# Performance work log

Measured on AMD Instinct MI355X. Metric: run time of the kernel, lower is better.

## Reference

```python
import jax, jax.numpy as jnp
import numpy as np

B, T = 256, 64
VOCAB = 10000
VIS, WORD, RNN = 1024, 512, 512


def setup_inputs() -> dict:
    key = jax.random.key(0)
    ks = jax.random.split(key, 12)
    s = 0.02
    return {
        "vis_feats": jax.random.normal(ks[0], (B, VIS), jnp.float32),
        "seqz": jax.random.randint(ks[1], (B, T), 0, VOCAB, jnp.int32),
        # learned params (x @ W convention, W: [in, out])
        "emb": jax.random.normal(ks[2], (VOCAB + 2, WORD), jnp.float32) * s,
        "W_ih": jax.random.normal(ks[3], (VIS + WORD, 4 * RNN), jnp.float32) * s,
        "W_hh": jax.random.normal(ks[4], (RNN, 4 * RNN), jnp.float32) * s,
        "b_lstm": jnp.zeros((4 * RNN,), jnp.float32),
        "vis2g_W": jax.random.normal(ks[5], (VIS, RNN), jnp.float32) * s,
        "vis2g_b": jnp.zeros((RNN,), jnp.float32),
        "w2g_W": jax.random.normal(ks[6], (WORD, RNN), jnp.float32) * s,
        "h2g_W": jax.random.normal(ks[7], (RNN, RNN), jnp.float32) * s,
        "out_W": jax.random.normal(ks[8], (RNN, VOCAB + 1), jnp.float32) * s,
        "out_b": jnp.zeros((VOCAB + 1,), jnp.float32),
    }


def _decode(vis_feats, seqz, emb, W_ih, W_hh, b_lstm, vis2g_W, vis2g_b,
            w2g_W, h2g_W, out_W, out_b):
    Bn, Tn = seqz.shape
    # input word ids per step: SOS (=vocab+1) at t=0, then seqz[:, t-1]
    sos = jnp.full((1, Bn), VOCAB + 1, seqz.dtype)
    words = jnp.concatenate([sos, seqz[:, :-1].T], axis=0)          # [T, B]
    mask = jnp.concatenate([jnp.ones((1, Bn), jnp.float32),
                            (seqz[:, :-1] != 0).T.astype(jnp.float32)], axis=0)  # [T, B]
    targets = seqz.T                                                 # [T, B]

    def step(carry, xs):
        h, c = carry
        widx, tgt, m = xs
        w = emb[widx]                                   # [B, 512]
        x = jnp.concatenate([vis_feats, w], axis=1)     # [B, 1536]
        gates = x @ W_ih + h @ W_hh + b_lstm            # [B, 2048]
        i_g, f_g, g_g, o_g = jnp.split(gates, 4, axis=1)
        c_new = jax.nn.sigmoid(f_g) * c + jax.nn.sigmoid(i_g) * jnp.tanh(g_g)
        h_new = jax.nn.sigmoid(o_g) * jnp.tanh(c_new)
        # visual-sentinel gate: g = sigmoid(w2g(w) + vis2g(vis) + h2g(h_prev))
        g = jax.nn.sigmoid(w @ w2g_W + vis_feats @ vis2g_W + vis2g_b + h @ h2g_W)
        s_t = g * jnp.tanh(c_new)                       # [B, 512]
        logits = s_t @ out_W + out_b                    # [B, V+1]
        lp = jax.nn.log_softmax(logits, axis=-1) * m[:, None]
        out_t = jnp.take_along_axis(lp, tgt[:, None], axis=1)[:, 0]  # [B]
        return (h_new, c_new), out_t

    init = (jnp.zeros((Bn, RNN), jnp.float32), jnp.zeros((Bn, RNN), jnp.float32))
    _, log_probs = jax.lax.scan(step, init, (words, targets, mask))
    return log_probs  # [T, B]


def reference(vis_feats, seqz, emb, W_ih, W_hh, b_lstm, vis2g_W, vis2g_b,
              w2g_W, h2g_W, out_W, out_b):
    return _decode(vis_feats, seqz, emb, W_ih, W_hh, b_lstm, vis2g_W,
                   vis2g_b, w2g_W, h2g_W, out_W, out_b)
```

## Files before the change

### kernel.cpp

```cpp
#include <hip/hip_runtime.h>
#include <hip/hip_bf16.h>
#include <math.h>

typedef __attribute__((ext_vector_type(8))) short short8;
typedef __attribute__((ext_vector_type(4))) float f32x4;

#define MFMA16(a, b, c) __builtin_amdgcn_mfma_f32_16x16x32_bf16((a), (b), (c), 0, 0, 0)

#define BB 256
#define TT 64
#define VOCAB 10000
#define WORD 512
#define RNN 512
#define NC 2560
#define NV 10001
#define NVP 10016
#define NTILES 626

typedef unsigned long long ull;
union U16 { ull u[2]; short8 s8; };

__device__ __forceinline__ float sigf(float x) { return 1.f / (1.f + __expf(-x)); }
__device__ __forceinline__ float bf2f(short s) {
    union { unsigned int u; float f; } v;
    v.u = ((unsigned int)(unsigned short)s) << 16;
    return v.f;
}
__device__ __forceinline__ short f2bfs(float x) {
    __hip_bfloat16 h = __float2bfloat16(x);
    return *reinterpret_cast<short*>(&h);
}

__device__ __forceinline__ void gload_lds16(const void* g, void* l) {
    __builtin_amdgcn_global_load_lds((const __attribute__((address_space(1))) void*)g,
                                     (__attribute__((address_space(3))) void*)l, 16, 0, 0);
}

__device__ __forceinline__ void stage_tile(const short8* gsrc, void* lbuf, int w, int lane) {
    const char* g = (const char*)gsrc + w * 4096 + lane * 16;
    char* l = (char*)lbuf + w * 4096;
#pragma unroll
    for (int i = 0; i < 4; i++) gload_lds16(g + i * 1024, l + i * 1024);
}


__global__ void transpose_cvt(const float* __restrict__ src, int K, int N, int ld,
                              __hip_bfloat16* __restrict__ dst, int dst_ld, int dstN) {
    __shared__ float tile[32][33];
    int k0 = blockIdx.y * 32, n0 = blockIdx.x * 32;
    int tx = threadIdx.x, ty = threadIdx.y;
#pragma unroll
    for (int i = 0; i < 32; i += 8) {
        int k = k0 + ty + i, n = n0 + tx;
        tile[ty + i][tx] = (k < K && n < N) ? src[(size_t)k * ld + n] : 0.f;
    }
    __syncthreads();
#pragma unroll
    for (int i = 0; i < 32; i += 8) {
        int n = n0 + ty + i, k = k0 + tx;
        if (n < dstN && k < K) dst[(size_t)n * dst_ld + k] = __float2bfloat16(tile[tx][ty + i]);
    }
}

__global__ void swizzle_frag(const short8* __restrict__ src, short8* __restrict__ dst, int ntiles) {
    int t = blockIdx.x * 256 + threadIdx.x;
    if (t >= ntiles * 1024) return;
    int ct = t >> 10, r = t & 1023, kt = r >> 6, l = r & 63;
    int li = l & 15, q = l >> 4;
    dst[t] = src[(size_t)(ct * 16 + li) * 64 + kt * 4 + q];
}

__global__ void zero_state(float* c, __hip_bfloat16* h) {
    int idx = blockIdx.x * 256 + threadIdx.x;
    c[idx] = 0.f;
    h[idx] = __float2bfloat16(0.f);
}

__global__ void cvt_vis(const float* __restrict__ v, __hip_bfloat16* __restrict__ d) {
    int idx = blockIdx.x * 256 + threadIdx.x;
    d[idx] = __float2bfloat16(v[idx]);
}

__global__ __launch_bounds__(256) void gemm_vis(const __hip_bfloat16* __restrict__ A,
                                                const __hip_bfloat16* __restrict__ Bt,
                                                const float* __restrict__ b_lstm,
                                                const float* __restrict__ vis2g_b,
                                                float* __restrict__ C) {
    int wid = blockIdx.x * 4 + (threadIdx.x >> 6);
    int mt = wid / 160, nt = wid % 160;
    int lane = threadIdx.x & 63, li = lane & 15, q = lane >> 4;
    const short8* Ap = (const short8*)A + (mt * 16 + li) * 128 + q;
    const short8* Bp = (const short8*)Bt + (nt * 16 + li) * 128 + q;
    f32x4 acc = {0.f, 0.f, 0.f, 0.f};
#pragma unroll
    for (int kk = 0; kk < 128; kk += 4) acc = MFMA16(Ap[kk], Bp[kk], acc);
    int col = nt * 16 + li;
    float bias = (col < 2048) ? b_lstm[col] : vis2g_b[col - 2048];
#pragma unroll
    for (int r = 0; r < 4; r++) {
        int row = mt * 16 + q * 4 + r;
        C[row * NC + col] = acc[r] + bias;
    }
}

__global__ __launch_bounds__(256) void pre_gemm(const int* __restrict__ seqz,
                                                const float* __restrict__ emb,
                                                const short8* __restrict__ Bsw,
                                                const float* __restrict__ visC,
                                                __hip_bfloat16* __restrict__ preF) {
    __shared__ short8 lds[2][1024];
    int w = threadIdx.x >> 6, lane = threadIdx.x & 63, li = lane & 15, q = lane >> 4;
    int r0 = blockIdx.x * 128 + w * 32;

    short8 a0[16], a1[16];
    {
        int row = r0 + li;
        int t = row >> 8, b = row & 255;
        int wid_ = (t == 0) ? (VOCAB + 1) : seqz[b * TT + (t - 1)];
        const float* er = emb + (size_t)wid_ * WORD + q * 8;
#pragma unroll
        for (int kt = 0; kt < 16; kt++) {
            float4 f0 = ((const float4*)(er + kt * 32))[0];
            float4 f1 = ((const float4*)(er + kt * 32))[1];
            short8 v; v[0]=f2bfs(f0.x); v[1]=f2bfs(f0.y); v[2]=f2bfs(f0.z); v[3]=f2bfs(f0.w);
            v[4]=f2bfs(f1.x); v[5]=f2bfs(f1.y); v[6]=f2bfs(f1.z); v[7]=f2bfs(f1.w);
            a0[kt] = v;
        }
        row = r0 + 16 + li; t = row >> 8; b = row & 255;
        wid_ = (t == 0) ? (VOCAB + 1) : seqz[b * TT + (t - 1)];
        er = emb + (size_t)wid_ * WORD + q * 8;
#pragma unroll
        for (int kt = 0; kt < 16; kt++) {
            float4 f0 = ((const float4*)(er + kt * 32))[0];
            float4 f1 = ((const float4*)(er + kt * 32))[1];
            short8 v; v[0]=f2bfs(f0.x); v[1]=f2bfs(f0.y); v[2]=f2bfs(f0.z); v[3]=f2bfs(f0.w);
            v[4]=f2bfs(f1.x); v[5]=f2bfs(f1.y); v[6]=f2bfs(f1.z); v[7]=f2bfs(f1.w);
            a1[kt] = v;
        }
    }

    int t0 = blockIdx.y * 20, t1 = t0 + 20;
    stage_tile(Bsw + (size_t)t0 * 1024, lds[0], w, lane);
    int ib = 0;
    for (int ct = t0; ct < t1; ++ct, ib ^= 1) {
        __syncthreads();
        if (ct + 1 < t1) stage_tile(Bsw + (size_t)(ct + 1) * 1024, lds[ib ^ 1], w, lane);
        const short8* B = lds[ib];
        f32x4 c0 = {0.f,0.f,0.f,0.f}, c1 = {0.f,0.f,0.f,0.f};
#pragma unroll
        for (int kt = 0; kt < 16; kt++) {
            short8 bv = B[kt * 64 + lane];
            c0 = MFMA16(bv, a0[kt], c0);
            c1 = MFMA16(bv, a1[kt], c1);
        }
        int col0 = ct * 16 + q * 4;
        size_t tb0 = ((size_t)(r0 >> 4) * 160 + ct) * 256 + lane * 4;
        size_t tb1 = tb0 + (size_t)160 * 256;
        float4 v0 = *(const float4*)(visC + ((r0 + li) & 255) * NC + col0);
        float4 v1 = *(const float4*)(visC + ((r0 + 16 + li) & 255) * NC + col0);
        preF[tb0 + 0] = __float2bfloat16(c0[0] + v0.x);
        preF[tb0 + 1] = __float2bfloat16(c0[1] + v0.y);
        preF[tb0 + 2] = __float2bfloat16(c0[2] + v0.z);
        preF[tb0 + 3] = __float2bfloat16(c0[3] + v0.w);
        preF[tb1 + 0] = __float2bfloat16(c1[0] + v1.x);
        preF[tb1 + 1] = __float2bfloat16(c1[1] + v1.y);
        preF[tb1 + 2] = __float2bfloat16(c1[2] + v1.z);
        preF[tb1 + 3] = __float2bfloat16(c1[3] + v1.w);
    }
}

__global__ __launch_bounds__(64, 1) void lstm_persist(const short8* __restrict__ WHsw,
                                                      const __hip_bfloat16* __restrict__ preF,
                                                      __hip_bfloat16* __restrict__ h0,
                                                      __hip_bfloat16* __restrict__ h1,
                                                      __hip_bfloat16* __restrict__ S,
                                                      int* __restrict__ flags) {
    __shared__ short8 ldsB[4096];
    int wid = blockIdx.x;
    int bt = wid & 15, jt = (wid >> 4) & 31;
    int lane = threadIdx.x;
    int li = lane & 15, q = lane >> 4;

#pragma unroll
    for (int g = 0; g < 4; ++g) {
        const char* src = (const char*)(WHsw + (size_t)(g * 32 + jt) * 1024) + lane * 16;
        char* dst = (char*)ldsB + g * 16384;
#pragma unroll
        for (int i = 0; i < 16; ++i) gload_lds16(src + i * 1024, dst + i * 1024);
    }
    short8 b4[16];
    const short8* B4 = WHsw + (size_t)(128 + jt) * 1024 + lane;
#pragma unroll
    for (int kt = 0; kt < 16; ++kt) b4[kt] = B4[kt * 64];
    __syncthreads();

    int* flagp = flags + bt * 64;
    f32x4 cacc = {0.f, 0.f, 0.f, 0.f};

    int hin  = (bt * 16 + li) * 1024 + q * 16;
    int hout = (bt * 16 + li) * 1024 + (jt * 16 + q * 4) * 2;

    const ull* ppw = (const ull*)preF + ((size_t)bt * 160 + jt) * 64 + lane;

    ull ppA[5], ppB[5];
#pragma unroll
    for (int g = 0; g < 5; ++g) ppA[g] = ppw[g * 2048];

#define LSTM_STEP(T, HC, HN, PPC, PPN)                                             \
  {                                                                                \
    if ((T) > 0) {                                                                 \
      int it = 0;                                                                  \
      while (true) {                                                               \
        int v = (T);                                                               \
        if (lane < 32)                                                             \
          v = __hip_atomic_load(flagp + lane, __ATOMIC_RELAXED,                    \
                                __HIP_MEMORY_SCOPE_SYSTEM);                        \
        if (__all(v >= (T))) break;                                                \
        if (++it > 30000) break;               \
        __builtin_amdgcn_s_sleep(1);                                               \
      }                                                                            \
    }                                                                              \
    const ull* hp = (const ull*)((const char*)(HC) + hin);                         \
    ull hf[32];                                                                    \
    _Pragma("unroll") for (int kt = 0; kt < 16; ++kt) {                            \
      hf[2 * kt]     = __hip_atomic_load(hp + kt * 8, __ATOMIC_RELAXED,            \
                                         __HIP_MEMORY_SCOPE_SYSTEM);               \
      hf[2 * kt + 1] = __hip_atomic_load(hp + kt * 8 + 1, __ATOMIC_RELAXED,        \
                                         __HIP_MEMORY_SCOPE_SYSTEM);               \
    }                                                                              \
    if ((T) + 1 < TT) {                                                            \
      const ull* pn = ppw + (size_t)((T) + 1) * 163840;                            \
      _Pragma("unroll") for (int g = 0; g < 5; ++g) (PPN)[g] = pn[g * 2048];       \
    }                                                                              \
    f32x4 g0 = {0.f, 0.f, 0.f, 0.f}, g1 = g0, g2 = g0, g3 = g0, g4 = g0;           \
    _Pragma("unroll") for (int kt = 0; kt < 16; ++kt) {                            \
      U16 hv; hv.u[0] = hf[2 * kt]; hv.u[1] = hf[2 * kt + 1];                      \
      short8 bv = hv.s8;                                                           \
      g0 = MFMA16(ldsB[       kt * 64 + lane], bv, g0);                            \
      g1 = MFMA16(ldsB[1024 + kt * 64 + lane], bv, g1);                            \
      g2 = MFMA16(ldsB[2048 + kt * 64 + lane], bv, g2);                            \
      g3 = MFMA16(ldsB[3072 + kt * 64 + lane], bv, g3);                            \
      g4 = MFMA16(b4[kt], bv, g4);                                                 \
    }                                                                              \
    ull hvout = 0ull, svout = 0ull;                                                \
    _Pragma("unroll") for (int r = 0; r < 4; ++r) {                                \
      float ig = sigf(g0[r] + bf2f((short)((PPC)[0] >> (16 * r))));                \
      float fg = sigf(g1[r] + bf2f((short)((PPC)[1] >> (16 * r))));                \
      float gg = tanhf(g2[r] + bf2f((short)((PPC)[2] >> (16 * r))));               \
      float og = sigf(g3[r] + bf2f((short)((PPC)[3] >> (16 * r))));                \
      float gp = sigf(g4[r] + bf2f((short)((PPC)[4] >> (16 * r))));                \
      float cn = fg * cacc[r] + ig * gg;                                           \
      float tc = tanhf(cn);                                                        \
      cacc[r] = cn;                                                                \
      hvout |= ((ull)(unsigned short)f2bfs(og * tc)) << (16 * r);                  \
      svout |= ((ull)(unsigned short)f2bfs(gp * tc)) << (16 * r);                  \
    }                                                                              \
    __hip_atomic_store((ull*)((char*)(HN) + hout), hvout,                          \
                       __ATOMIC_RELAXED, __HIP_MEMORY_SCOPE_SYSTEM);               \
    *(ull*)((char*)S + (size_t)(T) * 262144 + hout) = svout;                       \
    asm volatile("s_waitcnt vmcnt(0)" ::: "memory");                               \
    if (lane == 0)                                                                 \
      __hip_atomic_store(flagp + jt, (T) + 1, __ATOMIC_RELAXED,                    \
                         __HIP_MEMORY_SCOPE_SYSTEM);                               \
  }

    for (int t = 0; t < TT; t += 2) {
        LSTM_STEP(t,     h0, h1, ppA, ppB);
        LSTM_STEP(t + 1, h1, h0, ppB, ppA);
    }
#undef LSTM_STEP
}


__global__ __launch_bounds__(256) void lse_gemm(const short8* __restrict__ S8,
                                                const short8* __restrict__ Bsw,
                                                const float* __restrict__ ob,
                                                float* __restrict__ sumexp) {
    __shared__ short8 lds[2][1024];
    int w = threadIdx.x >> 6, lane = threadIdx.x & 63, li = lane & 15, q = lane >> 4;
    int r0 = blockIdx.x * 128 + w * 32;
    short8 a0[16], a1[16];
    const short8* Sp0 = S8 + (size_t)(r0 + li) * 64 + q;
    const short8* Sp1 = S8 + (size_t)(r0 + 16 + li) * 64 + q;
#pragma unroll
    for (int kt = 0; kt < 16; kt++) { a0[kt] = Sp0[kt * 4]; a1[kt] = Sp1[kt * 4]; }

    float s0[4] = {0.f,0.f,0.f,0.f}, s1[4] = {0.f,0.f,0.f,0.f};
    int t0 = blockIdx.y * 40;
    int t1 = t0 + 40 < NTILES ? t0 + 40 : NTILES;

    stage_tile(Bsw + (size_t)t0 * 1024, lds[0], w, lane);
    int ib = 0;
    for (int ct = t0; ct < t1; ++ct, ib ^= 1) {
        __syncthreads();
        if (ct + 1 < t1) stage_tile(Bsw + (size_t)(ct + 1) * 1024, lds[ib ^ 1], w, lane);
        const short8* B = lds[ib];
        f32x4 c0 = {0.f,0.f,0.f,0.f}, c1 = {0.f,0.f,0.f,0.f};
#pragma unroll
        for (int kt = 0; kt < 16; kt++) {
            short8 bv = B[kt * 64 + lane];
            c0 = MFMA16(a0[kt], bv, c0);
            c1 = MFMA16(a1[kt], bv, c1);
        }
        int col = ct * 16 + li;
        if (col < NV) {
            float obv = ob[col];
#pragma unroll
            for (int r = 0; r < 4; r++) {
                s0[r] += __expf(c0[r] + obv);
                s1[r] += __expf(c1[r] + obv);
            }
        }
    }
#pragma unroll
    for (int off = 1; off < 16; off <<= 1) {
#pragma unroll
        for (int r = 0; r < 4; r++) { s0[r] += __shfl_xor(s0[r], off); s1[r] += __shfl_xor(s1[r], off); }
    }
    if (li == 0) {
#pragma unroll
        for (int r = 0; r < 4; r++) {
            atomicAdd(&sumexp[r0 + q * 4 + r], s0[r]);
            atomicAdd(&sumexp[r0 + 16 + q * 4 + r], s1[r]);
        }
    }
}

__global__ __launch_bounds__(256) void finalize_k(const __hip_bfloat16* __restrict__ S,
                                                  const __hip_bfloat16* __restrict__ Wt,
                                                  const float* __restrict__ ob,
                                                  const int* __restrict__ seqz,
                                                  const float* __restrict__ sumexp,
                                                  float* __restrict__ out) {
    int w = threadIdx.x >> 6, lane = threadIdx.x & 63;
    int row = blockIdx.x * 4 + w;
    int t = row >> 8, b = row & 255;
    int tgt = seqz[b * TT + t];
    short8 sv = ((const short8*)(S + (size_t)row * 512))[lane];
    short8 wv = ((const short8*)(Wt + (size_t)tgt * 512))[lane];
    float d = 0.f;
#pragma unroll
    for (int i = 0; i < 8; i++) d += bf2f(sv[i]) * bf2f(wv[i]);
#pragma unroll
    for (int off = 1; off < 64; off <<= 1) d += __shfl_xor(d, off);
    if (lane == 0) {
        bool mk = (t == 0) || (seqz[b * TT + t - 1] != 0);
        out[row] = mk ? (d + ob[tgt] - logf(sumexp[row])) : 0.f;
    }
}


extern "C" void kernel_launch(void* const* d_in, const int* in_sizes, int n_in,
                              void* d_out, int out_size, void* d_ws, size_t ws_size,
                              hipStream_t stream) {
    const float* vis     = (const float*)d_in[0];
    const int*   seqz    = (const int*)d_in[1];
    const float* emb     = (const float*)d_in[2];
    const float* W_ih    = (const float*)d_in[3];
    const float* W_hh    = (const float*)d_in[4];
    const float* b_lstm  = (const float*)d_in[5];
    const float* vis2g_W = (const float*)d_in[6];
    const float* vis2g_b = (const float*)d_in[7];
    const float* w2g_W   = (const float*)d_in[8];
    const float* h2g_W   = (const float*)d_in[9];
    const float* out_W   = (const float*)d_in[10];
    const float* out_b   = (const float*)d_in[11];
    float* out = (float*)d_out;

    char* p = (char*)d_ws;
    auto carve = [&](size_t bytes) {
        void* r = (void*)p;
        p += (bytes + 255) & ~(size_t)255;
        return r;
    };
    __hip_bfloat16* WcatW = (__hip_bfloat16*)carve((size_t)NC * 512 * 2);
    __hip_bfloat16* WcatH = (__hip_bfloat16*)carve((size_t)NC * 512 * 2);
    __hip_bfloat16* visWt = (__hip_bfloat16*)carve((size_t)NC * 1024 * 2);
    __hip_bfloat16* outWt = (__hip_bfloat16*)carve((size_t)NVP * 512 * 2);
    short8*         outSw = (short8*)carve((size_t)NTILES * 16384);
    short8*         preBsw= (short8*)carve((size_t)160 * 16384);
    short8*         WHsw  = (short8*)carve((size_t)160 * 16384);
    __hip_bfloat16* visB  = (__hip_bfloat16*)carve((size_t)256 * 1024 * 2);
    float*          visC  = (float*)carve((size_t)256 * NC * 4);
    __hip_bfloat16* preF  = (__hip_bfloat16*)carve((size_t)TT * 256 * NC * 2);
    float*          cbuf  = (float*)carve((size_t)256 * 512 * 4);
    __hip_bfloat16* hb0   = (__hip_bfloat16*)carve((size_t)256 * 512 * 2);
    __hip_bfloat16* hb1   = (__hip_bfloat16*)carve((size_t)256 * 512 * 2);
    __hip_bfloat16* S     = (__hip_bfloat16*)carve((size_t)TT * 256 * 512 * 2);
    float*          sume  = (float*)carve((size_t)TT * 256 * 4);
    int*            bars  = (int*)carve((size_t)16 * 64 * 4);

    dim3 tb(32, 8);
    transpose_cvt<<<dim3(64, 16), tb, 0, stream>>>(W_ih + 1024 * 2048, 512, 2048, 2048, WcatW, 512, 2048);
    transpose_cvt<<<dim3(16, 16), tb, 0, stream>>>(w2g_W, 512, 512, 512, WcatW + 2048 * 512, 512, 512);
    transpose_cvt<<<dim3(64, 16), tb, 0, stream>>>(W_hh, 512, 2048, 2048, WcatH, 512, 2048);
    transpose_cvt<<<dim3(16, 16), tb, 0, stream>>>(h2g_W, 512, 512, 512, WcatH + 2048 * 512, 512, 512);
    transpose_cvt<<<dim3(64, 32), tb, 0, stream>>>(W_ih, 1024, 2048, 2048, visWt, 1024, 2048);
    transpose_cvt<<<dim3(16, 32), tb, 0, stream>>>(vis2g_W, 1024, 512, 512, visWt + 2048 * 1024, 1024, 512);
    transpose_cvt<<<dim3(313, 16), tb, 0, stream>>>(out_W, 512, NV, NV, outWt, 512, NVP);
    swizzle_frag<<<2504, 256, 0, stream>>>((const short8*)outWt, outSw, NTILES);
    swizzle_frag<<<640, 256, 0, stream>>>((const short8*)WcatW, preBsw, 160);
    swizzle_frag<<<640, 256, 0, stream>>>((const short8*)WcatH, WHsw, 160);

    zero_state<<<512, 256, 0, stream>>>(cbuf, hb0);
    cvt_vis<<<1024, 256, 0, stream>>>(vis, visB);
    gemm_vis<<<640, 256, 0, stream>>>(visB, visWt, b_lstm, vis2g_b, visC);
    pre_gemm<<<dim3(128, 8), 256, 0, stream>>>(seqz, emb, preBsw, visC, preF);

    hipMemsetAsync(sume, 0, (size_t)TT * 256 * 4, stream);
    hipMemsetAsync(bars, 0, (size_t)16 * 64 * 4, stream);

    {
        const short8* WHsw_c = (const short8*)WHsw;
        const __hip_bfloat16* preF_c = (const __hip_bfloat16*)preF;
        __hip_bfloat16* h0a = hb0;
        __hip_bfloat16* h1a = hb1;
        __hip_bfloat16* Sa = S;
        int* barsa = bars;
        void* kargs[6] = { &WHsw_c, &preF_c, &h0a, &h1a, &Sa, &barsa };
        hipLaunchCooperativeKernel((void*)lstm_persist, dim3(512), dim3(64), kargs, 0, stream);
    }

    lse_gemm<<<dim3(128, 16), 256, 0, stream>>>((const short8*)S, outSw, out_b, sume);
    finalize_k<<<4096, 256, 0, stream>>>(S, outWt, out_b, seqz, sume, out);
}
```

Baseline: 804.1 us.

## Pre-convert embeddings to bf16, use fast sigmoid/tanh, remap LSTM block indices

Adds a kernel that converts the whole embedding table to bf16 once, so pre_gemm loads bf16 rows directly instead of converting fp32 per row. The LSTM cell replaces the division and library tanh with hardware reciprocal-based approximations. It also changes the block-to-(batch tile, hidden tile) mapping in the persistent kernel, hoists the h fragment array out of the step macro with a compiler memory barrier, and replaces the zero_state kernel with memsets. The whole table conversion (about 10k rows) adds work compared with converting only the gathered rows, and the fast tanh may lose accuracy for large inputs.

```diff
diff --git a/kernel.cpp b/kernel.cpp
--- a/kernel.cpp
+++ b/kernel.cpp
@@ -20,7 +20,12 @@
 typedef unsigned long long ull;
 union U16 { ull u[2]; short8 s8; };
 
-__device__ __forceinline__ float sigf(float x) { return 1.f / (1.f + __expf(-x)); }
+__device__ __forceinline__ float sigf(float x) {
+    return __builtin_amdgcn_rcpf(1.f + __expf(-x));
+}
+__device__ __forceinline__ float tanhf_fast(float x) {
+    return 1.f - 2.f * __builtin_amdgcn_rcpf(__expf(2.f * x) + 1.f);
+}
 __device__ __forceinline__ float bf2f(short s) {
     union { unsigned int u; float f; } v;
     v.u = ((unsigned int)(unsigned short)s) << 16;
@@ -70,15 +75,20 @@
     dst[t] = src[(size_t)(ct * 16 + li) * 64 + kt * 4 + q];
 }
 
-__global__ void zero_state(float* c, __hip_bfloat16* h) {
-    int idx = blockIdx.x * 256 + threadIdx.x;
-    c[idx] = 0.f;
-    h[idx] = __float2bfloat16(0.f);
-}
-
 __global__ void cvt_vis(const float* __restrict__ v, __hip_bfloat16* __restrict__ d) {
     int idx = blockIdx.x * 256 + threadIdx.x;
     d[idx] = __float2bfloat16(v[idx]);
+}
+
+__global__ void cvt_emb(const float* __restrict__ e, short8* __restrict__ d, int n8) {
+    int idx = blockIdx.x * 256 + threadIdx.x;
+    if (idx >= n8) return;
+    const float4* s = (const float4*)e + (size_t)idx * 2;
+    float4 f0 = s[0], f1 = s[1];
+    short8 v;
+    v[0]=f2bfs(f0.x); v[1]=f2bfs(f0.y); v[2]=f2bfs(f0.z); v[3]=f2bfs(f0.w);
+    v[4]=f2bfs(f1.x); v[5]=f2bfs(f1.y); v[6]=f2bfs(f1.z); v[7]=f2bfs(f1.w);
+    d[idx] = v;
 }
 
 __global__ __launch_bounds__(256) void gemm_vis(const __hip_bfloat16* __restrict__ A,
@@ -104,7 +114,7 @@
 }
 
 __global__ __launch_bounds__(256) void pre_gemm(const int* __restrict__ seqz,
-                                                const float* __restrict__ emb,
+                                                const __hip_bfloat16* __restrict__ embB,
                                                 const short8* __restrict__ Bsw,
                                                 const float* __restrict__ visC,
                                                 __hip_bfloat16* __restrict__ preF) {
@@ -117,26 +127,14 @@
         int row = r0 + li;
         int t = row >> 8, b = row & 255;
         int wid_ = (t == 0) ? (VOCAB + 1) : seqz[b * TT + (t - 1)];
-        const float* er = emb + (size_t)wid_ * WORD + q * 8;
-#pragma unroll
-        for (int kt = 0; kt < 16; kt++) {
-            float4 f0 = ((const float4*)(er + kt * 32))[0];
-            float4 f1 = ((const float4*)(er + kt * 32))[1];
-            short8 v; v[0]=f2bfs(f0.x); v[1]=f2bfs(f0.y); v[2]=f2bfs(f0.z); v[3]=f2bfs(f0.w);
-            v[4]=f2bfs(f1.x); v[5]=f2bfs(f1.y); v[6]=f2bfs(f1.z); v[7]=f2bfs(f1.w);
-            a0[kt] = v;
-        }
+        const short8* er = (const short8*)(embB + (size_t)wid_ * WORD) + q;
+#pragma unroll
+        for (int kt = 0; kt < 16; kt++) a0[kt] = er[kt * 4];
         row = r0 + 16 + li; t = row >> 8; b = row & 255;
         wid_ = (t == 0) ? (VOCAB + 1) : seqz[b * TT + (t - 1)];
-        er = emb + (size_t)wid_ * WORD + q * 8;
-#pragma unroll
-        for (int kt = 0; kt < 16; kt++) {
-            float4 f0 = ((const float4*)(er + kt * 32))[0];
-            float4 f1 = ((const float4*)(er + kt * 32))[1];
-            short8 v; v[0]=f2bfs(f0.x); v[1]=f2bfs(f0.y); v[2]=f2bfs(f0.z); v[3]=f2bfs(f0.w);
-            v[4]=f2bfs(f1.x); v[5]=f2bfs(f1.y); v[6]=f2bfs(f1.z); v[7]=f2bfs(f1.w);
-            a1[kt] = v;
-        }
+        er = (const short8*)(embB + (size_t)wid_ * WORD) + q;
+#pragma unroll
+        for (int kt = 0; kt < 16; kt++) a1[kt] = er[kt * 4];
     }
 
     int t0 = blockIdx.y * 20, t1 = t0 + 20;
@@ -177,7 +175,7 @@
                                                       int* __restrict__ flags) {
     __shared__ short8 ldsB[4096];
     int wid = blockIdx.x;
-    int bt = wid & 15, jt = (wid >> 4) & 31;
+    int bt = wid >> 5, jt = wid & 31;
     int lane = threadIdx.x;
     int li = lane & 15, q = lane >> 4;
 
@@ -205,6 +203,8 @@
     ull ppA[5], ppB[5];
 #pragma unroll
     for (int g = 0; g < 5; ++g) ppA[g] = ppw[g * 2048];
+
+    ull hf[32];
 
 #define LSTM_STEP(T, HC, HN, PPC, PPN)                                             \
   {                                                                                \
@@ -220,8 +220,8 @@
         __builtin_amdgcn_s_sleep(1);                                               \
       }                                                                            \
     }                                                                              \
+    asm volatile("" ::: "memory");        \
     const ull* hp = (const ull*)((const char*)(HC) + hin);                         \
-    ull hf[32];                                                                    \
     _Pragma("unroll") for (int kt = 0; kt < 16; ++kt) {                            \
       hf[2 * kt]     = __hip_atomic_load(hp + kt * 8, __ATOMIC_RELAXED,            \
                                          __HIP_MEMORY_SCOPE_SYSTEM);               \
@@ -246,11 +246,11 @@
     _Pragma("unroll") for (int r = 0; r < 4; ++r) {                                \
       float ig = sigf(g0[r] + bf2f((short)((PPC)[0] >> (16 * r))));                \
       float fg = sigf(g1[r] + bf2f((short)((PPC)[1] >> (16 * r))));                \
-      float gg = tanhf(g2[r] + bf2f((short)((PPC)[2] >> (16 * r))));               \
+      float gg = tanhf_fast(g2[r] + bf2f((short)((PPC)[2] >> (16 * r))));          \
       float og = sigf(g3[r] + bf2f((short)((PPC)[3] >> (16 * r))));                \
       float gp = sigf(g4[r] + bf2f((short)((PPC)[4] >> (16 * r))));                \
       float cn = fg * cacc[r] + ig * gg;                                           \
-      float tc = tanhf(cn);                                                        \
+      float tc = tanhf_fast(cn);                                                   \
       cacc[r] = cn;                                                                \
       hvout |= ((ull)(unsigned short)f2bfs(og * tc)) << (16 * r);                  \
       svout |= ((ull)(unsigned short)f2bfs(gp * tc)) << (16 * r);                  \
@@ -381,9 +381,9 @@
     short8*         preBsw= (short8*)carve((size_t)160 * 16384);
     short8*         WHsw  = (short8*)carve((size_t)160 * 16384);
     __hip_bfloat16* visB  = (__hip_bfloat16*)carve((size_t)256 * 1024 * 2);
+    __hip_bfloat16* embB  = (__hip_bfloat16*)carve((size_t)(VOCAB + 2) * WORD * 2);
     float*          visC  = (float*)carve((size_t)256 * NC * 4);
     __hip_bfloat16* preF  = (__hip_bfloat16*)carve((size_t)TT * 256 * NC * 2);
-    float*          cbuf  = (float*)carve((size_t)256 * 512 * 4);
     __hip_bfloat16* hb0   = (__hip_bfloat16*)carve((size_t)256 * 512 * 2);
     __hip_bfloat16* hb1   = (__hip_bfloat16*)carve((size_t)256 * 512 * 2);
     __hip_bfloat16* S     = (__hip_bfloat16*)carve((size_t)TT * 256 * 512 * 2);
@@ -402,13 +402,14 @@
     swizzle_frag<<<640, 256, 0, stream>>>((const short8*)WcatW, preBsw, 160);
     swizzle_frag<<<640, 256, 0, stream>>>((const short8*)WcatH, WHsw, 160);
 
-    zero_state<<<512, 256, 0, stream>>>(cbuf, hb0);
+    hipMemsetAsync(hb0, 0, (size_t)256 * 512 * 2, stream);
+    hipMemsetAsync(bars, 0, (size_t)16 * 64 * 4, stream);
+    hipMemsetAsync(sume, 0, (size_t)TT * 256 * 4, stream);
+
     cvt_vis<<<1024, 256, 0, stream>>>(vis, visB);
+    cvt_emb<<<2501, 256, 0, stream>>>(emb, (short8*)embB, (VOCAB + 2) * WORD / 8);
     gemm_vis<<<640, 256, 0, stream>>>(visB, visWt, b_lstm, vis2g_b, visC);
-    pre_gemm<<<dim3(128, 8), 256, 0, stream>>>(seqz, emb, preBsw, visC, preF);
-
-    hipMemsetAsync(sume, 0, (size_t)TT * 256 * 4, stream);
-    hipMemsetAsync(bars, 0, (size_t)16 * 64 * 4, stream);
+    pre_gemm<<<dim3(128, 8), 256, 0, stream>>>(seqz, embB, preBsw, visC, preF);
 
     {
         const short8* WHsw_c = (const short8*)WHsw;
```

Measured after the change: 750.1 us. 1.07x faster.
